# Performance work log

Hardware: AMD Instinct MI355X
Metric: run time of the kernel (lower is better)

The kernel has to match this reference:

```python
import jax, jax.numpy as jnp
import numpy as np

B, S, E, H = 4, 4096, 512, 64


def setup_inputs() -> dict:
    key = jax.random.key(0)
    ks = jax.random.split(key, 6)
    query = jax.random.normal(ks[0], (B, S, E), dtype=jnp.float32)
    key_t = jax.random.normal(ks[1], (B, S, E), dtype=jnp.float32)
    value = jax.random.normal(ks[2], (B, S, E), dtype=jnp.float32)
    # nn.Linear weights are [out, in] = [H, E]; biases [H]
    Wq = jax.random.normal(ks[3], (H, E), dtype=jnp.float32) * 0.02
    Wk = jax.random.normal(ks[4], (H, E), dtype=jnp.float32) * 0.02
    Wv = jax.random.normal(ks[5], (H, E), dtype=jnp.float32) * 0.02
    bq = jnp.zeros((H,), jnp.float32)
    bk = jnp.zeros((H,), jnp.float32)
    bv = jnp.zeros((H,), jnp.float32)
    # causal mask, broadcast over batch; masked_fill where mask == 0
    mask = jnp.tril(jnp.ones((1, S, S), dtype=jnp.bool_))
    return {"query": query, "key": key_t, "value": value,
            "Wq": Wq, "bq": bq, "Wk": Wk, "bk": bk, "Wv": Wv, "bv": bv,
            "mask": mask}


def reference(query, key, value, Wq, bq, Wk, bk, Wv, bv, mask):
    # Bug-faithful: d_k is the LAST dim of the *input* query, i.e. embed_dim
    d_k = query.shape[-1]
    q = jnp.einsum('bse,he->bsh', query, Wq) + bq   # [B,S,H]
    k = jnp.einsum('bse,he->bsh', key, Wk) + bk     # [B,S,H]
    v = jnp.einsum('bse,he->bsh', value, Wv) + bv   # [B,S,H]
    scores = jnp.einsum('bqh,bkh->bqk', q, k) / jnp.sqrt(jnp.float32(d_k))  # [B,S,S]
    scores = jnp.where(mask, scores, -jnp.inf)
    weights = jax.nn.softmax(scores, axis=-1)
    # dropout_rate = 0.0 -> Dropout is identity
    out = jnp.einsum('bqk,bkh->bqh', weights, v)    # [B,S,H]
    return out
```

## Files before the change

kernel.cpp:

```cpp
#include <hip/hip_runtime.h>
#include <hip/hip_bf16.h>
#include <math.h>

typedef unsigned short u16;
typedef unsigned int   u32;
typedef __attribute__((ext_vector_type(8)))  short bf16x8_t;
typedef __attribute__((ext_vector_type(4)))  float f32x4_t;
typedef __attribute__((ext_vector_type(16))) float f32x16_t;
typedef __attribute__((ext_vector_type(4)))  int   i32x4_t;
typedef __attribute__((ext_vector_type(2)))  u32   u32x2_t;

#define SEQ 4096
#define EMB 512
#define HD  64
#define NBATCH 4
#define C2 0.063758718f

#define NPAIR 136
#define SLOTS (NBATCH * NPAIR * 8)

__device__ __forceinline__ u16 to_bf(float f) {
    __hip_bfloat16 h = __float2bfloat16(f);
    return __builtin_bit_cast(u16, h);
}

__device__ __forceinline__ void stage16(const void* g, void* l) {
    __builtin_amdgcn_global_load_lds(
        (const __attribute__((address_space(1))) void*)g,
        (__attribute__((address_space(3))) void*)l, 16, 0, 0);
}

__global__ __launch_bounds__(256)
void wprep_kernel(const float* __restrict__ Wq, const float* __restrict__ Wk,
                  const float* __restrict__ Wv, u16* __restrict__ wbf)
{
    const int zkt = blockIdx.x;
    const int z   = zkt >> 4;
    const int kt  = zkt & 15;
    const float* W = (z == 0) ? Wq : (z == 1) ? Wk : Wv;
    const int kn   = threadIdx.x >> 6;
    const int lane = threadIdx.x & 63;
    const int l15  = lane & 15;
    const int lg   = lane >> 4;

    const float* src = W + (size_t)(kn * 16 + l15) * EMB + kt * 32 + lg * 8;
    f32x4_t f0 = *reinterpret_cast<const f32x4_t*>(src);
    f32x4_t f1 = *reinterpret_cast<const f32x4_t*>(src + 4);
    u16 tmp[8];
    #pragma unroll
    for (int e = 0; e < 4; ++e) { tmp[e] = to_bf(f0[e]); tmp[4 + e] = to_bf(f1[e]); }
    *reinterpret_cast<i32x4_t*>(
        &wbf[((size_t)((z * 16 + kt) * 4 + kn)) * 512 + lane * 8]) =
        *reinterpret_cast<const i32x4_t*>(tmp);
}

__global__ __launch_bounds__(256, 3)
void proj_kernel(const float* __restrict__ q_in, const float* __restrict__ k_in,
                 const float* __restrict__ v_in, const u16* __restrict__ wbf,
                 const float* __restrict__ bq, const float* __restrict__ bk,
                 const float* __restrict__ bv,
                 u16* __restrict__ outQ, u16* __restrict__ outK,
                 u16* __restrict__ outVT)
{
    const int z = blockIdx.y;
    const float* in   = (z == 0) ? q_in : (z == 1) ? k_in : v_in;
    const float* bias = (z == 0) ? bq   : (z == 1) ? bk   : bv;

    const int tid  = threadIdx.x;
    const int lane = tid & 63;
    const int w    = tid >> 6;
    const int l15  = lane & 15;
    const int lg   = lane >> 4;
    const int g0   = blockIdx.x * 64;
    const int row  = g0 + w * 16 + l15;

    const float* arow = in + (size_t)row * EMB + lg * 8;
    const u16*   wz   = wbf + (size_t)z * 16 * 4 * 512 + lane * 8;

    float bvals[4];
    #pragma unroll
    for (int kn = 0; kn < 4; ++kn) bvals[kn] = bias[kn * 16 + l15];
    asm volatile("" :: "v"(bvals[0]), "v"(bvals[1]), "v"(bvals[2]), "v"(bvals[3]));

    f32x4_t acc[4];
    #pragma unroll
    for (int i = 0; i < 4; ++i)
        #pragma unroll
        for (int j = 0; j < 4; ++j) acc[i][j] = 0.f;

    f32x4_t  a0[4], a1[4];
    bf16x8_t wf[4][4];

#define ISSUE(kt)                                                              \
    {                                                                          \
        a0[(kt) & 3] = *reinterpret_cast<const f32x4_t*>(arow + (kt) * 32);    \
        a1[(kt) & 3] = *reinterpret_cast<const f32x4_t*>(arow + (kt) * 32 + 4);\
        _Pragma("unroll")                                                      \
        for (int kn = 0; kn < 4; ++kn)                                         \
            wf[(kt) & 3][kn] = *reinterpret_cast<const bf16x8_t*>(             \
                wz + ((size_t)((kt) * 4 + kn) << 9));                          \
    }

    #pragma unroll
    for (int kt = 0; kt < 4; ++kt) ISSUE(kt);

    #pragma unroll
    for (int kt = 0; kt < 16; ++kt) {
        const int s = kt & 3;
        u16 ta[8];
        #pragma unroll
        for (int e = 0; e < 4; ++e) { ta[e] = to_bf(a0[s][e]); ta[4 + e] = to_bf(a1[s][e]); }
        bf16x8_t af = *reinterpret_cast<const bf16x8_t*>(ta);
        #pragma unroll
        for (int kn = 0; kn < 4; ++kn)
            acc[kn] = __builtin_amdgcn_mfma_f32_16x16x32_bf16(af, wf[s][kn], acc[kn], 0, 0, 0);
        if (kt < 12) ISSUE(kt + 4);
    }
#undef ISSUE

    #pragma unroll
    for (int kn = 0; kn < 4; ++kn) {
        const int col = kn * 16 + l15;
        #pragma unroll
        for (int j = 0; j < 4; ++j) {
            const int grow = g0 + w * 16 + lg * 4 + j;
            const u16 val = to_bf(acc[kn][j] + bvals[kn]);
            if (z == 0) {
                outQ[(size_t)grow * HD + col] = val;
            } else if (z == 1) {
                outK[(size_t)grow * HD + col] = val;
            } else {
                const int b = grow >> 12, s2 = grow & (SEQ - 1);
                outVT[((size_t)(b * HD + col)) * SEQ + s2] = val;
            }
        }
    }
}

__global__ __launch_bounds__(512, 4)
void attn8_kernel(const u16* __restrict__ Q, const u16* __restrict__ K,
                  const u16* __restrict__ VT,
                  u16* __restrict__ partO, float* __restrict__ partL)
{
    __shared__ u16 Kt[2][64 * 64];
    __shared__ u16 Vt[2][64 * 64];
    __shared__ u16 Pt[8][32 * 64];

    const int tid  = threadIdx.x;
    const int w    = tid >> 6;
    const int lane = tid & 63;
    const int q31  = lane & 31;
    const int half = lane >> 5;

    const int b = blockIdx.y;
    const int y = blockIdx.x;
    int g = 0;
    while ((g + 1) * (g + 2) / 2 <= y) ++g;
    const int c = y - g * (g + 1) / 2;

    const int R0   = 256 * g + 32 * w;
    const int q_g  = R0 + q31;
    const int nt_w = 4 * g + (w >> 1) + 1;
    const int t0   = 4 * c, t1 = 4 * c + 4;

    const u16* Kb  = K  + (size_t)b * SEQ * HD;
    const u16* VTb = VT + (size_t)b * HD * SEQ;

    const int srow = w * 8 + (lane >> 3);
    const int schk = (lane & 7) ^ ((lane >> 3) & 7);

    bf16x8_t qf0, qf1, qf2, qf3;
    {
        const u16* qp = Q + ((size_t)b * SEQ + q_g) * HD + 8 * half;
        qf0 = *(const bf16x8_t*)(qp + 0);
        qf1 = *(const bf16x8_t*)(qp + 16);
        qf2 = *(const bf16x8_t*)(qp + 32);
        qf3 = *(const bf16x8_t*)(qp + 48);
    }

    f32x16_t acc0, acc1;
    #pragma unroll
    for (int i = 0; i < 16; ++i) { acc0[i] = 0.f; acc1[i] = 0.f; }
    float lsum = 0.f;

    auto STAGE = [&](int u, int t) {
        stage16(&Kb[((size_t)(t * 64 + srow)) * HD + schk * 8], &Kt[u][w * 512]);
        stage16(&VTb[(size_t)srow * SEQ + t * 64 + schk * 8],   &Vt[u][w * 512]);
    };

    STAGE(0, t0);
    asm volatile("s_waitcnt vmcnt(0)" ::: "memory");
    __syncthreads();

    for (int t = t0; t < t1; ++t) {
        const int u = (t - t0) & 1;
        if (t + 1 < t1) STAGE(u ^ 1, t + 1);
        if (t < nt_w) {
            const bool last = (t == nt_w - 1);
            #pragma unroll
            for (int ksub = 0; ksub < 2; ++ksub) {
                f32x16_t sf;
                #pragma unroll
                for (int i = 0; i < 16; ++i) sf[i] = 0.f;
                const int kl = ksub * 32 + q31;
                #pragma unroll
                for (int s = 0; s < 4; ++s) {
                    bf16x8_t a = *(const bf16x8_t*)
                        &Kt[u][kl * 64 + ((s * 16 + 8 * half) ^ ((kl & 7) << 3))];
                    bf16x8_t qq = (s == 0) ? qf0 : (s == 1) ? qf1 : (s == 2) ? qf2 : qf3;
                    sf = __builtin_amdgcn_mfma_f32_32x32x16_bf16(a, qq, sf, 0, 0, 0);
                }
                #pragma unroll
                for (int j = 0; j < 4; ++j) {
                    float p[4];
                    #pragma unroll
                    for (int e = 0; e < 4; ++e) {
                        const int kk    = 8 * j + 4 * half + e;
                        const int key_g = t * 64 + ksub * 32 + kk;
                        float v = exp2f(sf[4 * j + e] * C2);
                        if (last && key_g > q_g) v = 0.f;
                        lsum += v;
                        p[e] = v;
                    }
                    u32x2_t pk;
                    pk[0] = (u32)to_bf(p[0]) | ((u32)to_bf(p[1]) << 16);
                    pk[1] = (u32)to_bf(p[2]) | ((u32)to_bf(p[3]) << 16);
                    const int col = (ksub * 32 + 8 * j + 4 * half) ^ ((q31 & 7) << 3);
                    *(u32x2_t*)&Pt[w][q31 * 64 + col] = pk;
                }
            }
            asm volatile("s_waitcnt lgkmcnt(0)" ::: "memory");
            __builtin_amdgcn_sched_barrier(0);
            #pragma unroll
            for (int kp = 0; kp < 4; ++kp) {
                bf16x8_t pb = *(const bf16x8_t*)
                    &Pt[w][q31 * 64 + ((kp * 16 + 8 * half) ^ ((q31 & 7) << 3))];
                {
                    const int dl = q31;
                    bf16x8_t va = *(const bf16x8_t*)
                        &Vt[u][dl * 64 + ((kp * 16 + 8 * half) ^ ((dl & 7) << 3))];
                    acc0 = __builtin_amdgcn_mfma_f32_32x32x16_bf16(va, pb, acc0, 0, 0, 0);
                }
                {
                    const int dl = 32 + q31;
                    bf16x8_t va = *(const bf16x8_t*)
                        &Vt[u][dl * 64 + ((kp * 16 + 8 * half) ^ ((dl & 7) << 3))];
                    acc1 = __builtin_amdgcn_mfma_f32_32x32x16_bf16(va, pb, acc1, 0, 0, 0);
                }
            }
        }
        asm volatile("s_waitcnt vmcnt(0)" ::: "memory");
        __syncthreads();
    }

    lsum += __shfl_xor(lsum, 32);
    const int slot = (b * NPAIR + y) * 8 + w;
    u16* po = partO + (size_t)slot * 2048;
    #pragma unroll
    for (int dsub = 0; dsub < 2; ++dsub) {
        #pragma unroll
        for (int j = 0; j < 4; ++j) {
            const f32x16_t& a = dsub ? acc1 : acc0;
            u32x2_t pk;
            pk[0] = (u32)to_bf(a[4 * j + 0]) | ((u32)to_bf(a[4 * j + 1]) << 16);
            pk[1] = (u32)to_bf(a[4 * j + 2]) | ((u32)to_bf(a[4 * j + 3]) << 16);
            const int d = 32 * dsub + 8 * j + 4 * half;
            *(u32x2_t*)&po[q31 * 64 + d] = pk;
        }
    }
    if (half == 0) partL[(size_t)slot * 32 + q31] = lsum;
}

__global__ __launch_bounds__(256)
void reduce8_kernel(const u16* __restrict__ partO, const float* __restrict__ partL,
                    float* __restrict__ out)
{
    const int x  = blockIdx.x;
    const int b  = x >> 7;
    const int gw = x & 127;
    const int g  = gw >> 3;
    const int w  = gw & 7;
    const int ybase = g * (g + 1) / 2;

    const int t  = threadIdx.x;
    const int q  = t >> 3;
    const int d0 = (t & 7) * 8;

    float acc[8];
    #pragma unroll
    for (int i = 0; i < 8; ++i) acc[i] = 0.f;
    float l = 0.f;

    for (int c = 0; c <= g; ++c) {
        const int slot = (b * NPAIR + ybase + c) * 8 + w;
        i32x4_t raw = *(const i32x4_t*)(partO + (size_t)slot * 2048 + q * 64 + d0);
        const u16* pr = (const u16*)&raw;
        #pragma unroll
        for (int i = 0; i < 8; ++i) {
            u32 bits = ((u32)pr[i]) << 16;
            acc[i] += __builtin_bit_cast(float, bits);
        }
        l += partL[(size_t)slot * 32 + q];
    }
    const float inv = 1.f / l;
    f32x4_t r0, r1;
    #pragma unroll
    for (int i = 0; i < 4; ++i) { r0[i] = acc[i] * inv; r1[i] = acc[4 + i] * inv; }
    const size_t row = (size_t)b * SEQ + g * 256 + w * 32 + q;
    *(f32x4_t*)&out[row * HD + d0]     = r0;
    *(f32x4_t*)&out[row * HD + d0 + 4] = r1;
}

extern "C" void kernel_launch(void* const* d_in, const int* in_sizes, int n_in,
                              void* d_out, int out_size, void* d_ws, size_t ws_size,
                              hipStream_t stream)
{
    const float* q_in = (const float*)d_in[0];
    const float* k_in = (const float*)d_in[1];
    const float* v_in = (const float*)d_in[2];
    const float* Wq   = (const float*)d_in[3];
    const float* bq   = (const float*)d_in[4];
    const float* Wk   = (const float*)d_in[5];
    const float* bk   = (const float*)d_in[6];
    const float* Wv   = (const float*)d_in[7];
    const float* bv   = (const float*)d_in[8];
    float* out = (float*)d_out;

    const size_t NQ = (size_t)NBATCH * SEQ * HD;
    u16* wsQ   = (u16*)d_ws;
    u16* wsK   = wsQ + NQ;
    u16* wsVT  = wsK + NQ;
    u16* partO = wsVT + NQ;
    float* partL = (float*)(partO + (size_t)SLOTS * 2048);
    u16* wbf = partO;

    wprep_kernel<<<dim3(48), 256, 0, stream>>>(Wq, Wk, Wv, wbf);
    proj_kernel<<<dim3(256, 3), 256, 0, stream>>>(q_in, k_in, v_in, wbf,
                                                  bq, bk, bv, wsQ, wsK, wsVT);
    attn8_kernel<<<dim3(NPAIR, NBATCH), 512, 0, stream>>>(wsQ, wsK, wsVT, partO, partL);
    reduce8_kernel<<<dim3(512), 256, 0, stream>>>(partO, partL, out);
}
```

Baseline: 72.05 us.

## Stage projection input tiles through swizzled LDS with async global-to-LDS loads

```diff
diff --git a/kernel.cpp b/kernel.cpp
--- a/kernel.cpp
+++ b/kernel.cpp
@@ -54,7 +54,7 @@
         *reinterpret_cast<const i32x4_t*>(tmp);
 }
 
-__global__ __launch_bounds__(256, 3)
+__global__ __launch_bounds__(256)
 void proj_kernel(const float* __restrict__ q_in, const float* __restrict__ k_in,
                  const float* __restrict__ v_in, const u16* __restrict__ wbf,
                  const float* __restrict__ bq, const float* __restrict__ bk,
@@ -66,54 +66,64 @@
     const float* in   = (z == 0) ? q_in : (z == 1) ? k_in : v_in;
     const float* bias = (z == 0) ? bq   : (z == 1) ? bk   : bv;
 
+    __shared__ __align__(16) float A_lds[4][4][16][32];
+
     const int tid  = threadIdx.x;
     const int lane = tid & 63;
     const int w    = tid >> 6;
     const int l15  = lane & 15;
     const int lg   = lane >> 4;
     const int g0   = blockIdx.x * 64;
-    const int row  = g0 + w * 16 + l15;
-
-    const float* arow = in + (size_t)row * EMB + lg * 8;
-    const u16*   wz   = wbf + (size_t)z * 16 * 4 * 512 + lane * 8;
+
+    const u16* wz = wbf + (size_t)z * 16 * 4 * 512 + lane * 8;
 
     float bvals[4];
     #pragma unroll
     for (int kn = 0; kn < 4; ++kn) bvals[kn] = bias[kn * 16 + l15];
     asm volatile("" :: "v"(bvals[0]), "v"(bvals[1]), "v"(bvals[2]), "v"(bvals[3]));
 
+    const int sr = lane >> 3;
+    const int sc = (lane & 7) ^ (sr & 7);
+    const float* abase = in + (size_t)(g0 + w * 16 + sr) * EMB + sc * 4;
+
+#define ISSUE(kt)                                                               \
+    {                                                                           \
+        stage16(abase +            (kt) * 32, &A_lds[(kt) & 3][w][0][0]);       \
+        stage16(abase + 8 * EMB +  (kt) * 32, &A_lds[(kt) & 3][w][8][0]);       \
+    }
+
     f32x4_t acc[4];
     #pragma unroll
     for (int i = 0; i < 4; ++i)
         #pragma unroll
         for (int j = 0; j < 4; ++j) acc[i][j] = 0.f;
 
-    f32x4_t  a0[4], a1[4];
-    bf16x8_t wf[4][4];
-
-#define ISSUE(kt)                                                              \
-    {                                                                          \
-        a0[(kt) & 3] = *reinterpret_cast<const f32x4_t*>(arow + (kt) * 32);    \
-        a1[(kt) & 3] = *reinterpret_cast<const f32x4_t*>(arow + (kt) * 32 + 4);\
-        _Pragma("unroll")                                                      \
-        for (int kn = 0; kn < 4; ++kn)                                         \
-            wf[(kt) & 3][kn] = *reinterpret_cast<const bf16x8_t*>(             \
-                wz + ((size_t)((kt) * 4 + kn) << 9));                          \
-    }
-
-    #pragma unroll
-    for (int kt = 0; kt < 4; ++kt) ISSUE(kt);
+    const int rsw = l15 & 7;
+    const int p0  = (lg * 2) ^ rsw;
+
+    ISSUE(0); ISSUE(1); ISSUE(2); ISSUE(3);
 
     #pragma unroll
     for (int kt = 0; kt < 16; ++kt) {
+        if (kt <= 12)      asm volatile("s_waitcnt vmcnt(6)" ::: "memory");
+        else if (kt == 13) asm volatile("s_waitcnt vmcnt(4)" ::: "memory");
+        else if (kt == 14) asm volatile("s_waitcnt vmcnt(2)" ::: "memory");
+        else               asm volatile("s_waitcnt vmcnt(0)" ::: "memory");
+        __builtin_amdgcn_sched_barrier(0);
+
         const int s = kt & 3;
+        f32x4_t a0 = *reinterpret_cast<const f32x4_t*>(&A_lds[s][w][l15][p0 * 4]);
+        f32x4_t a1 = *reinterpret_cast<const f32x4_t*>(&A_lds[s][w][l15][(p0 ^ 1) * 4]);
         u16 ta[8];
         #pragma unroll
-        for (int e = 0; e < 4; ++e) { ta[e] = to_bf(a0[s][e]); ta[4 + e] = to_bf(a1[s][e]); }
+        for (int e = 0; e < 4; ++e) { ta[e] = to_bf(a0[e]); ta[4 + e] = to_bf(a1[e]); }
         bf16x8_t af = *reinterpret_cast<const bf16x8_t*>(ta);
         #pragma unroll
-        for (int kn = 0; kn < 4; ++kn)
-            acc[kn] = __builtin_amdgcn_mfma_f32_16x16x32_bf16(af, wf[s][kn], acc[kn], 0, 0, 0);
+        for (int kn = 0; kn < 4; ++kn) {
+            bf16x8_t wfrag = *reinterpret_cast<const bf16x8_t*>(
+                wz + ((size_t)(kt * 4 + kn) << 9));
+            acc[kn] = __builtin_amdgcn_mfma_f32_16x16x32_bf16(af, wfrag, acc[kn], 0, 0, 0);
+        }
         if (kt < 12) ISSUE(kt + 4);
     }
 #undef ISSUE
```

Result: no change. 70.67 us (-1.9%).
